# Optimization experiments

Hardware: AMD Instinct MI355X
Metric: run time of the kernel (lower is better)

The kernel has to match this reference:

```python
import jax, jax.numpy as jnp
import numpy as np

H, W = 4096, 4096
KH, KW = 15, 15


def setup_inputs() -> dict:
    key = jax.random.key(0)
    k1, k2 = jax.random.split(key)
    X = jax.random.normal(k1, (H, W), dtype=jnp.float32)
    weight = jax.random.uniform(k2, (KH, KW), dtype=jnp.float32)
    bias = jnp.zeros((1,), dtype=jnp.float32)
    return {"X": X, "weight": weight, "bias": bias}


def reference(X, weight, bias):
    # 2D cross-correlation, 'valid' padding: out[i,j] = sum(X[i:i+kh, j:j+kw] * K) + b
    lhs = X[None, None, :, :]                 # [1,1,H,W]
    rhs = weight[None, None, :, :]            # [1,1,KH,KW] (cross-correlation: no flip)
    out = jax.lax.conv_general_dilated(
        lhs, rhs,
        window_strides=(1, 1),
        padding="VALID",
        dimension_numbers=("NCHW", "OIHW", "NCHW"),
    )[0, 0]                                   # [H-KH+1, W-KW+1]
    return out + bias[0]
```

## Files before the change

### kernel.cpp

```cpp
#include <hip/hip_runtime.h>
#include <hip/hip_bf16.h>


#define IN_DIM   4096
#define OUT_DIM  4082
#define KDIM     15
#define BM       128
#define BN       112
#define SLAB_R   142
#define SLAB_C   128
#define NTX      7

typedef __attribute__((ext_vector_type(8))) short  short8;
typedef __attribute__((ext_vector_type(4))) float  f32x4;

__global__ __launch_bounds__(256) void conv15_mfma(
    const float* __restrict__ X, const float* __restrict__ Wt,
    const float* __restrict__ bias, float* __restrict__ out) {
  __shared__ __align__(16) unsigned short sX[SLAB_R * SLAB_C];
  __shared__ __align__(16) unsigned short sB[KDIM * 16 * 32];

  const int tid = threadIdx.x;
  const int x0 = blockIdx.x * BN;
  const int y0 = blockIdx.y * BM;

  for (int idx = tid; idx < KDIM * 512; idx += 256) {
    const int ky = idx >> 9;
    const int n  = (idx >> 5) & 15;
    const int k  = idx & 31;
    const int kx = k - n;
    unsigned short v = 0;
    if (kx >= 0 && kx < KDIM) {
      __hip_bfloat16 h = __float2bfloat16(Wt[ky * KDIM + kx]);
      v = *reinterpret_cast<const unsigned short*>(&h);
    }
    sB[idx] = v;
  }

  for (int idx = tid; idx < SLAB_R * (SLAB_C / 8); idx += 256) {
    const int r  = idx >> 4;
    const int c8 = (idx & 15) << 3;
    const int gr = y0 + r;
    const int gc = x0 + c8;
    float f[8];
    if (gr < IN_DIM && gc + 7 < IN_DIM) {
      const float* p = X + (size_t)gr * IN_DIM + gc;
      const f32x4 a = *reinterpret_cast<const f32x4*>(p);
      const f32x4 b = *reinterpret_cast<const f32x4*>(p + 4);
      f[0] = a.x; f[1] = a.y; f[2] = a.z; f[3] = a.w;
      f[4] = b.x; f[5] = b.y; f[6] = b.z; f[7] = b.w;
    } else {
#pragma unroll
      for (int j = 0; j < 8; ++j)
        f[j] = (gr < IN_DIM && gc + j < IN_DIM)
                 ? X[(size_t)gr * IN_DIM + gc + j] : 0.f;
    }
    short8 pk;
#pragma unroll
    for (int j = 0; j < 8; ++j) {
      __hip_bfloat16 h = __float2bfloat16(f[j]);
      pk[j] = *reinterpret_cast<const short*>(&h);
    }
    const int byte = (r * (SLAB_C * 2) + c8 * 2) ^ ((r & 7) << 4);
    *reinterpret_cast<short8*>(reinterpret_cast<char*>(sX) + byte) = pk;
  }
  __syncthreads();

  const int lane = tid & 63;
  const int wv   = tid >> 6;
  const int m    = lane & 15;
  const int g    = lane >> 4;

  f32x4 acc[2][NTX];
#pragma unroll
  for (int a = 0; a < 2; ++a)
#pragma unroll
    for (int b = 0; b < NTX; ++b)
      acc[a][b] = (f32x4){0.f, 0.f, 0.f, 0.f};

#pragma unroll 1
  for (int ky = 0; ky < KDIM; ++ky) {
    const short8 bfrag = *reinterpret_cast<const short8*>(
        reinterpret_cast<const char*>(sB) + ky * 1024 + m * 64 + g * 16);
#pragma unroll
    for (int ty = 0; ty < 2; ++ty) {
      const int r = (2 * wv + ty) * 16 + m + ky;
      const int rowbyte = r * (SLAB_C * 2);
      const int sw = (r & 7) << 4;
#pragma unroll
      for (int xt = 0; xt < NTX; ++xt) {
        const int byte = (rowbyte + (xt * 16 + g * 8) * 2) ^ sw;
        const short8 afrag = *reinterpret_cast<const short8*>(
            reinterpret_cast<const char*>(sX) + byte);
        acc[ty][xt] = __builtin_amdgcn_mfma_f32_16x16x32_bf16(
            afrag, bfrag, acc[ty][xt], 0, 0, 0);
      }
    }
  }

  const float bv = bias[0];
#pragma unroll
  for (int ty = 0; ty < 2; ++ty) {
    const int gy0 = y0 + (2 * wv + ty) * 16 + g * 4;
#pragma unroll
    for (int xt = 0; xt < NTX; ++xt) {
      const int ox = x0 + xt * 16 + m;
      if (ox < OUT_DIM) {
#pragma unroll
        for (int q = 0; q < 4; ++q) {
          const int oy = gy0 + q;
          if (oy < OUT_DIM)
            out[(size_t)oy * OUT_DIM + ox] = acc[ty][xt][q] + bv;
        }
      }
    }
  }
}

extern "C" void kernel_launch(void* const* d_in, const int* in_sizes, int n_in,
                              void* d_out, int out_size, void* d_ws, size_t ws_size,
                              hipStream_t stream) {
  const float* X    = (const float*)d_in[0];
  const float* Wt   = (const float*)d_in[1];
  const float* bias = (const float*)d_in[2];
  float* out = (float*)d_out;

  dim3 grid((OUT_DIM + BN - 1) / BN,
            (OUT_DIM + BM - 1) / BM);
  conv15_mfma<<<grid, 256, 0, stream>>>(X, Wt, bias, out);
}
```

Before: 146.5 us.

## Shrink tile width, drop LDS swizzle, preload weights, fully unroll ky loop

Narrows the output tile from 112 to 96 columns so the bf16 input slab takes 120 columns (240-byte rows) with no XOR swizzle, cutting LDS per block. It sets launch bounds to allow three blocks per CU and loads all 15 weight fragments into registers once. The ky loop is fully unrolled with fixed base pointers. Global loads clamp indices instead of branching. The cost is more blocks, more halo re-reads, possible LDS bank conflicts from the unswizzled 240-byte stride, and higher register pressure.

Measured after the change: 142.1 us. -3.0%, faster.

```diff
diff --git a/kernel.cpp b/kernel.cpp
--- a/kernel.cpp
+++ b/kernel.cpp
@@ -6,18 +6,20 @@
 #define OUT_DIM  4082
 #define KDIM     15
 #define BM       128
-#define BN       112
+#define BN       96
+#define NTX      6
 #define SLAB_R   142
-#define SLAB_C   128
-#define NTX      7
+#define SLAB_CE  120
+#define SLAB_CB  240
+#define SLAB_CH  15
 
 typedef __attribute__((ext_vector_type(8))) short  short8;
 typedef __attribute__((ext_vector_type(4))) float  f32x4;
 
-__global__ __launch_bounds__(256) void conv15_mfma(
+__global__ __launch_bounds__(256, 3) void conv15_mfma(
     const float* __restrict__ X, const float* __restrict__ Wt,
     const float* __restrict__ bias, float* __restrict__ out) {
-  __shared__ __align__(16) unsigned short sX[SLAB_R * SLAB_C];
+  __shared__ __align__(16) unsigned short sX[SLAB_R * SLAB_CE];
   __shared__ __align__(16) unsigned short sB[KDIM * 16 * 32];
 
   const int tid = threadIdx.x;
@@ -37,32 +39,23 @@
     sB[idx] = v;
   }
 
-  for (int idx = tid; idx < SLAB_R * (SLAB_C / 8); idx += 256) {
-    const int r  = idx >> 4;
-    const int c8 = (idx & 15) << 3;
-    const int gr = y0 + r;
-    const int gc = x0 + c8;
-    float f[8];
-    if (gr < IN_DIM && gc + 7 < IN_DIM) {
-      const float* p = X + (size_t)gr * IN_DIM + gc;
-      const f32x4 a = *reinterpret_cast<const f32x4*>(p);
-      const f32x4 b = *reinterpret_cast<const f32x4*>(p + 4);
-      f[0] = a.x; f[1] = a.y; f[2] = a.z; f[3] = a.w;
-      f[4] = b.x; f[5] = b.y; f[6] = b.z; f[7] = b.w;
-    } else {
-#pragma unroll
-      for (int j = 0; j < 8; ++j)
-        f[j] = (gr < IN_DIM && gc + j < IN_DIM)
-                 ? X[(size_t)gr * IN_DIM + gc + j] : 0.f;
-    }
+  for (int idx = tid; idx < SLAB_R * SLAB_CH; idx += 256) {
+    const int r = idx / SLAB_CH;
+    const int c = idx - r * SLAB_CH;
+    int gr = y0 + r;           if (gr > IN_DIM - 1) gr = IN_DIM - 1;
+    int gc = x0 + c * 8;       if (gc > IN_DIM - 8) gc = IN_DIM - 8;
+    const float* p = X + (size_t)gr * IN_DIM + gc;
+    const f32x4 a = *reinterpret_cast<const f32x4*>(p);
+    const f32x4 b = *reinterpret_cast<const f32x4*>(p + 4);
+    float f[8] = {a.x, a.y, a.z, a.w, b.x, b.y, b.z, b.w};
     short8 pk;
 #pragma unroll
     for (int j = 0; j < 8; ++j) {
       __hip_bfloat16 h = __float2bfloat16(f[j]);
       pk[j] = *reinterpret_cast<const short*>(&h);
     }
-    const int byte = (r * (SLAB_C * 2) + c8 * 2) ^ ((r & 7) << 4);
-    *reinterpret_cast<short8*>(reinterpret_cast<char*>(sX) + byte) = pk;
+    *reinterpret_cast<short8*>(
+        reinterpret_cast<char*>(sX) + r * SLAB_CB + c * 16) = pk;
   }
   __syncthreads();
 
@@ -71,6 +64,12 @@
   const int m    = lane & 15;
   const int g    = lane >> 4;
 
+  short8 bf[KDIM];
+#pragma unroll
+  for (int ky = 0; ky < KDIM; ++ky)
+    bf[ky] = *reinterpret_cast<const short8*>(
+        reinterpret_cast<const char*>(sB) + ky * 1024 + m * 64 + g * 16);
+
   f32x4 acc[2][NTX];
 #pragma unroll
   for (int a = 0; a < 2; ++a)
@@ -78,23 +77,25 @@
     for (int b = 0; b < NTX; ++b)
       acc[a][b] = (f32x4){0.f, 0.f, 0.f, 0.f};
 
-#pragma unroll 1
+  const char* base0 = reinterpret_cast<const char*>(sX)
+                    + (32 * wv + m) * SLAB_CB + 16 * g;
+  const char* base1 = base0 + 16 * SLAB_CB;
+
+#pragma unroll
   for (int ky = 0; ky < KDIM; ++ky) {
-    const short8 bfrag = *reinterpret_cast<const short8*>(
-        reinterpret_cast<const char*>(sB) + ky * 1024 + m * 64 + g * 16);
 #pragma unroll
-    for (int ty = 0; ty < 2; ++ty) {
-      const int r = (2 * wv + ty) * 16 + m + ky;
-      const int rowbyte = r * (SLAB_C * 2);
-      const int sw = (r & 7) << 4;
+    for (int xt = 0; xt < NTX; ++xt) {
+      const short8 a0 = *reinterpret_cast<const short8*>(
+          base0 + ky * SLAB_CB + 32 * xt);
+      acc[0][xt] = __builtin_amdgcn_mfma_f32_16x16x32_bf16(
+          a0, bf[ky], acc[0][xt], 0, 0, 0);
+    }
 #pragma unroll
-      for (int xt = 0; xt < NTX; ++xt) {
-        const int byte = (rowbyte + (xt * 16 + g * 8) * 2) ^ sw;
-        const short8 afrag = *reinterpret_cast<const short8*>(
-            reinterpret_cast<const char*>(sX) + byte);
-        acc[ty][xt] = __builtin_amdgcn_mfma_f32_16x16x32_bf16(
-            afrag, bfrag, acc[ty][xt], 0, 0, 0);
-      }
+    for (int xt = 0; xt < NTX; ++xt) {
+      const short8 a1 = *reinterpret_cast<const short8*>(
+          base1 + ky * SLAB_CB + 32 * xt);
+      acc[1][xt] = __builtin_amdgcn_mfma_f32_16x16x32_bf16(
+          a1, bf[ky], acc[1][xt], 0, 0, 0);
     }
   }
 
```
